# Performance work log

Measured on AMD Instinct MI355X. Metric: run time of the kernel, lower is better.

The kernel has to match this reference:

```python
import jax, jax.numpy as jnp
import numpy as np

EMBED_DIM = 2048
HEAD_DIM = 128
B, T = 4, 2048


def setup_inputs() -> dict:
    key = jax.random.key(0)
    k1, k2, k3, k4 = jax.random.split(key, 4)
    x_in = jax.random.normal(k1, (B, T, EMBED_DIM), dtype=jnp.float32)
    scale = 1.0 / np.sqrt(EMBED_DIM)
    Wq = jax.random.normal(k2, (EMBED_DIM, HEAD_DIM), dtype=jnp.float32) * scale
    Wk = jax.random.normal(k3, (EMBED_DIM, HEAD_DIM), dtype=jnp.float32) * scale
    Wv = jax.random.normal(k4, (EMBED_DIM, HEAD_DIM), dtype=jnp.float32) * scale
    return {"x_in": x_in, "Wq": Wq, "Wk": Wk, "Wv": Wv}


def reference(x_in, Wq, Wk, Wv):
    # x_in: [B, T, E]; projections (Linear, no bias)
    q = jnp.einsum('bte,ed->btd', x_in, Wq)  # [B,T,D]
    k = jnp.einsum('bte,ed->btd', x_in, Wk)
    v = jnp.einsum('bte,ed->btd', x_in, Wv)
    t = x_in.shape[1]
    d = Wq.shape[1]
    s = jnp.einsum('btd,bsd->bts', q, k) / jnp.sqrt(jnp.asarray(d, q.dtype))  # [B,Tq,Tk]
    # causal mask: positions with tril==0 (k index > q index) -> -inf
    causal = jnp.tril(jnp.ones((t, t), dtype=bool))
    s = jnp.where(causal, s, -jnp.inf)
    # NOTE: original module applies softmax over dim=1 (query axis), faithfully reproduced
    a = jax.nn.softmax(s, axis=1)
    z = jnp.einsum('bts,bsd->btd', a, v)  # [B,T,D]
    return z
```

## Files before the change

### kernel.cpp

```cpp
#include <hip/hip_runtime.h>

typedef _Float16 f16x8 __attribute__((ext_vector_type(8)));
typedef float f32x4 __attribute__((ext_vector_type(4)));

#define T_DIM 2048
#define E_DIM 2048
#define D_DIM 128
#define NB 4
#define CHUNK 32
#define NCH (T_DIM / CHUNK)
#define KSP 4
#define KCH 512

__device__ __forceinline__ void gll16(const void* g, void* l) {
  __builtin_amdgcn_global_load_lds(
      (const __attribute__((address_space(1))) unsigned int*)g,
      (__attribute__((address_space(3))) unsigned int*)l, 16, 0, 0);
}


__global__ void cvt_x(const float* __restrict__ x, _Float16* __restrict__ xh) {
  size_t i = ((size_t)blockIdx.x * 256 + threadIdx.x) * 8;
  f32x4 a = *(const f32x4*)(x + i);
  f32x4 b = *(const f32x4*)(x + i + 4);
  f16x8 o;
#pragma unroll
  for (int e = 0; e < 4; ++e) { o[e] = (_Float16)a[e]; o[e + 4] = (_Float16)b[e]; }
  *(f16x8*)(xh + i) = o;
}

__global__ void cvt_w(const float* __restrict__ Wq, const float* __restrict__ Wk,
                      const float* __restrict__ Wv, _Float16* __restrict__ WhT) {
  int idx = blockIdx.x * 256 + threadIdx.x;
  int w = blockIdx.y;
  const float* W = (w == 0) ? Wq : ((w == 1) ? Wk : Wv);
  int e = idx & (E_DIM - 1), d = idx >> 11;
  WhT[(size_t)w * (D_DIM * E_DIM) + idx] = (_Float16)W[e * D_DIM + d];
}


__global__ __launch_bounds__(256) void proj_gemm(
    const _Float16* __restrict__ xh, const _Float16* __restrict__ WhT,
    _Float16* __restrict__ Ph) {
  __shared__ _Float16 As[128 * 32];
  __shared__ _Float16 Bs[128 * 32];
  const int tid = threadIdx.x, w = tid >> 6, lane = tid & 63;
  const int wr = w >> 1, wc = w & 1, quad = lane >> 4, l16 = lane & 15;
  const int t0 = blockIdx.x * 128;
  const int wsel = blockIdx.y, ks = blockIdx.z;
  const _Float16* A = xh;
  const _Float16* B = WhT + (size_t)wsel * (D_DIM * E_DIM);
  const int srow = lane >> 2, scol = (lane & 3) * 8;
  f32x4 acc[4][4] = {};
  for (int k0 = ks * KCH; k0 < ks * KCH + KCH; k0 += 32) {
    __syncthreads();
#pragma unroll
    for (int q = 0; q < 2; ++q) {
      int rbase = w * 32 + q * 16;
      gll16(A + (size_t)(t0 + rbase + srow) * E_DIM + k0 + scol, As + rbase * 32);
      gll16(B + (size_t)(rbase + srow) * E_DIM + k0 + scol, Bs + rbase * 32);
    }
    __syncthreads();
    f16x8 af[4], bf[4];
#pragma unroll
    for (int i = 0; i < 4; ++i)
      af[i] = *(const f16x8*)(As + (wr * 64 + i * 16 + l16) * 32 + quad * 8);
#pragma unroll
    for (int j = 0; j < 4; ++j)
      bf[j] = *(const f16x8*)(Bs + (wc * 64 + j * 16 + l16) * 32 + quad * 8);
#pragma unroll
    for (int i = 0; i < 4; ++i)
#pragma unroll
      for (int j = 0; j < 4; ++j)
        acc[i][j] = __builtin_amdgcn_mfma_f32_16x16x32_f16(af[i], bf[j], acc[i][j], 0, 0, 0);
  }
  _Float16* P = Ph + ((size_t)(ks * 3 + wsel) << 20);
#pragma unroll
  for (int i = 0; i < 4; ++i)
#pragma unroll
    for (int j = 0; j < 4; ++j) {
      int n = wc * 64 + j * 16 + l16;
#pragma unroll
      for (int r = 0; r < 4; ++r) {
        int t = t0 + wr * 64 + i * 16 + quad * 4 + r;
        _Float16 h = (_Float16)acc[i][j][r];
        if (wsel < 2) P[(size_t)t * D_DIM + n] = h;
        else P[((size_t)(t >> 11) * D_DIM + n) * T_DIM + (t & (T_DIM - 1))] = h;
      }
    }
}


__global__ void proj_reduce(const _Float16* __restrict__ Ph, _Float16* __restrict__ Qh,
                            _Float16* __restrict__ Kh, _Float16* __restrict__ VT) {
  size_t u = ((size_t)blockIdx.x * 256 + threadIdx.x) * 8;
  int mat = (int)(u >> 20);
  size_t rem = u & ((1u << 20) - 1);
  float s[8] = {};
#pragma unroll
  for (int ks = 0; ks < KSP; ++ks) {
    f16x8 p = *(const f16x8*)(Ph + ((size_t)(ks * 3 + mat) << 20) + rem);
#pragma unroll
    for (int e = 0; e < 8; ++e) s[e] += (float)p[e];
  }
  f16x8 o;
#pragma unroll
  for (int e = 0; e < 8; ++e) o[e] = (_Float16)s[e];
  _Float16* dst = (mat == 0) ? Qh : ((mat == 1) ? Kh : VT);
  *(f16x8*)(dst + rem) = o;
}


__global__ __launch_bounds__(256) void s_gemm(const _Float16* __restrict__ Qh,
                                              const _Float16* __restrict__ Kh,
                                              _Float16* __restrict__ S) {
  if (blockIdx.y > blockIdx.x) return;
  __shared__ _Float16 As[128 * 32];
  __shared__ _Float16 Bs[128 * 32];
  const int tid = threadIdx.x, w = tid >> 6, lane = tid & 63;
  const int wr = w >> 1, wc = w & 1, quad = lane >> 4, l16 = lane & 15;
  const int t0 = blockIdx.x * 128, s0 = blockIdx.y * 128, b = blockIdx.z;
  const _Float16* A = Qh + (size_t)b * T_DIM * D_DIM;
  const _Float16* B = Kh + (size_t)b * T_DIM * D_DIM;
  const int srow = lane >> 2, scol = (lane & 3) * 8;
  f32x4 acc[4][4] = {};
  for (int k0 = 0; k0 < D_DIM; k0 += 32) {
    __syncthreads();
#pragma unroll
    for (int q = 0; q < 2; ++q) {
      int rbase = w * 32 + q * 16;
      gll16(A + (size_t)(t0 + rbase + srow) * D_DIM + k0 + scol, As + rbase * 32);
      gll16(B + (size_t)(s0 + rbase + srow) * D_DIM + k0 + scol, Bs + rbase * 32);
    }
    __syncthreads();
    f16x8 af[4], bf[4];
#pragma unroll
    for (int i = 0; i < 4; ++i)
      af[i] = *(const f16x8*)(As + (wr * 64 + i * 16 + l16) * 32 + quad * 8);
#pragma unroll
    for (int j = 0; j < 4; ++j)
      bf[j] = *(const f16x8*)(Bs + (wc * 64 + j * 16 + l16) * 32 + quad * 8);
#pragma unroll
    for (int i = 0; i < 4; ++i)
#pragma unroll
      for (int j = 0; j < 4; ++j)
        acc[i][j] = __builtin_amdgcn_mfma_f32_16x16x32_f16(af[i], bf[j], acc[i][j], 0, 0, 0);
  }
  _Float16* Sb = S + (size_t)b * T_DIM * T_DIM;
  const float scale = 0.08838834764831845f;
#pragma unroll
  for (int i = 0; i < 4; ++i)
#pragma unroll
    for (int j = 0; j < 4; ++j) {
      int s = s0 + wc * 64 + j * 16 + l16;
#pragma unroll
      for (int r = 0; r < 4; ++r) {
        int t = t0 + wr * 64 + i * 16 + quad * 4 + r;
        float v = acc[i][j][r] * scale;
        _Float16 h = (s > t) ? (_Float16)(-__builtin_inff()) : (_Float16)v;
        Sb[(size_t)t * T_DIM + s] = h;
      }
    }
}


__global__ __launch_bounds__(256) void part_stats(const _Float16* __restrict__ S,
                                                  float* __restrict__ Pm,
                                                  float* __restrict__ Pl) {
  const int ch = blockIdx.x, b = blockIdx.y;
  const int tbase = ch * CHUNK;
  const int s = blockIdx.z * 256 + threadIdx.x;
  const _Float16* Sb = S + (size_t)b * T_DIM * T_DIM;
  float m = -__builtin_inff(), l = 0.f;
  if (tbase + CHUNK - 1 >= s) {
    float v[CHUNK];
#pragma unroll
    for (int r = 0; r < CHUNK; ++r) {
      int t = tbase + r;
      v[r] = (t >= s) ? (float)Sb[(size_t)t * T_DIM + s] : -__builtin_inff();
      m = fmaxf(m, v[r]);
    }
#pragma unroll
    for (int r = 0; r < CHUNK; ++r) l += __expf(v[r] - m);
  }
  Pm[((size_t)ch * NB + b) * T_DIM + s] = m;
  Pl[((size_t)ch * NB + b) * T_DIM + s] = l;
}


__device__ __forceinline__ void merge_stat(float& m, float& l, float pm, float pl) {
  if (pm != -__builtin_inff()) {
    float nm = fmaxf(m, pm);
    l = l * __expf(m - nm) + pl * __expf(pm - nm);
    m = nm;
  }
}

__global__ __launch_bounds__(256) void comb_stats(const float* __restrict__ Pm,
                                                  const float* __restrict__ Pl,
                                                  float* __restrict__ M,
                                                  float* __restrict__ L) {
  __shared__ float sM[8][32];
  __shared__ float sL[8][32];
  const int g = threadIdx.x >> 5, sl = threadIdx.x & 31;
  const int c = blockIdx.x * 32 + sl;
  const int b = c >> 11, s = c & (T_DIM - 1);
  float m = -__builtin_inff(), l = 0.f;
#pragma unroll
  for (int k = 0; k < NCH / 8; ++k) {
    int ch = g * 8 + k;
    if (ch * CHUNK + CHUNK - 1 >= s) {
      size_t idx = ((size_t)ch * NB + b) * T_DIM + s;
      merge_stat(m, l, Pm[idx], Pl[idx]);
    }
  }
  sM[g][sl] = m;
  sL[g][sl] = l;
  __syncthreads();
  if (threadIdx.x < 32) {
    const int c2 = blockIdx.x * 32 + threadIdx.x;
    float fm = -__builtin_inff(), fl = 0.f;
#pragma unroll
    for (int gg = 0; gg < 8; ++gg) merge_stat(fm, fl, sM[gg][threadIdx.x], sL[gg][threadIdx.x]);
    M[c2] = fm;
    L[c2] = 1.f / fl;
  }
}


__global__ __launch_bounds__(256) void av_gemm(const _Float16* __restrict__ S,
                                               const _Float16* __restrict__ VT,
                                               const float* __restrict__ M,
                                               const float* __restrict__ L,
                                               float* __restrict__ Zp) {
  const int t0 = blockIdx.x * 128, b = blockIdx.y, ks = blockIdx.z;
  const int Kmax = t0 + 128;
  const int Kstart = ks * KCH;
  if (Kstart >= Kmax) return;
  const int Kend = (Kstart + KCH < Kmax) ? (Kstart + KCH) : Kmax;
  __shared__ _Float16 As[128 * 32];
  __shared__ _Float16 Bs[128 * 32];
  __shared__ float Ms[KCH];
  __shared__ float Ls[KCH];
  const int tid = threadIdx.x, w = tid >> 6, lane = tid & 63;
  const int wr = w >> 1, wc = w & 1, quad = lane >> 4, l16 = lane & 15;
  const _Float16* Sb = S + (size_t)b * T_DIM * T_DIM;
  const _Float16* Vb = VT + (size_t)b * D_DIM * T_DIM;
  for (int i = tid; i < Kend - Kstart; i += 256) {
    Ms[i] = M[b * T_DIM + Kstart + i];
    Ls[i] = L[b * T_DIM + Kstart + i];
  }
  const int srow = lane >> 2, scol = (lane & 3) * 8;
  f32x4 acc[4][4] = {};
  for (int k0 = Kstart; k0 < Kend; k0 += 32) {
    __syncthreads();
#pragma unroll
    for (int q = 0; q < 2; ++q) {
      int u = q * 256 + tid;
      int row = u >> 2, c8 = (u & 3) * 8;
      int sc = k0 + c8;
      f16x8 v = *(const f16x8*)(Sb + (size_t)(t0 + row) * T_DIM + sc);
      f16x8 o;
#pragma unroll
      for (int e = 0; e < 8; ++e) {
        int li = sc + e - Kstart;
        float a = __expf((float)v[e] - Ms[li]) * Ls[li];
        o[e] = (_Float16)a;
      }
      *(f16x8*)(As + row * 32 + c8) = o;
      int rbase = w * 32 + q * 16;
      gll16(Vb + (size_t)(rbase + srow) * T_DIM + k0 + scol, Bs + rbase * 32);
    }
    __syncthreads();
    f16x8 af[4], bf[4];
#pragma unroll
    for (int i = 0; i < 4; ++i)
      af[i] = *(const f16x8*)(As + (wr * 64 + i * 16 + l16) * 32 + quad * 8);
#pragma unroll
    for (int j = 0; j < 4; ++j)
      bf[j] = *(const f16x8*)(Bs + (wc * 64 + j * 16 + l16) * 32 + quad * 8);
#pragma unroll
    for (int i = 0; i < 4; ++i)
#pragma unroll
      for (int j = 0; j < 4; ++j)
        acc[i][j] = __builtin_amdgcn_mfma_f32_16x16x32_f16(af[i], bf[j], acc[i][j], 0, 0, 0);
  }
  float* Zb = Zp + (((size_t)ks * NB + b) * T_DIM) * D_DIM;
#pragma unroll
  for (int i = 0; i < 4; ++i)
#pragma unroll
    for (int j = 0; j < 4; ++j) {
      int n = wc * 64 + j * 16 + l16;
#pragma unroll
      for (int r = 0; r < 4; ++r) {
        int t = t0 + wr * 64 + i * 16 + quad * 4 + r;
        Zb[(size_t)t * D_DIM + n] = acc[i][j][r];
      }
    }
}


__global__ void z_reduce(const float* __restrict__ Zp, float* __restrict__ Z) {
  size_t flat = ((size_t)blockIdx.x * 256 + threadIdx.x) * 4;
  int t = (int)((flat >> 7) & (T_DIM - 1));
  int ns = ((t >> 7) + 4) >> 2;
  f32x4 s = {};
  for (int ks = 0; ks < ns; ++ks) {
    f32x4 p = *(const f32x4*)(Zp + ((size_t)ks * NB * T_DIM * D_DIM) + flat);
    s += p;
  }
  *(f32x4*)(Z + flat) = s;
}


extern "C" void kernel_launch(void* const* d_in, const int* in_sizes, int n_in,
                              void* d_out, int out_size, void* d_ws, size_t ws_size,
                              hipStream_t stream) {
  const float* x = (const float*)d_in[0];
  const float* Wq = (const float*)d_in[1];
  const float* Wk = (const float*)d_in[2];
  const float* Wv = (const float*)d_in[3];
  char* ws = (char*)d_ws;
  _Float16* xh = (_Float16*)(ws);
  float* Zp = (float*)(ws);
  _Float16* WhT = (_Float16*)(ws + 33554432);
  _Float16* Qh = (_Float16*)(ws + 35127296);
  _Float16* Kh = (_Float16*)(ws + 37224448);
  _Float16* VT = (_Float16*)(ws + 39321600);
  _Float16* S = (_Float16*)(ws + 41418752);
  _Float16* Ph = (_Float16*)(ws + 41418752);
  float* M = (float*)(ws + 74973184);
  float* L = (float*)(ws + 75005952);
  float* Pm = (float*)(ws + 75038720);
  float* Pl = (float*)(ws + 77135872);
  float* Z = (float*)d_out;

  cvt_x<<<8192, 256, 0, stream>>>(x, xh);
  cvt_w<<<dim3(1024, 3), 256, 0, stream>>>(Wq, Wk, Wv, WhT);
  proj_gemm<<<dim3(64, 3, KSP), 256, 0, stream>>>(xh, WhT, Ph);
  proj_reduce<<<1536, 256, 0, stream>>>(Ph, Qh, Kh, VT);
  s_gemm<<<dim3(16, 16, 4), 256, 0, stream>>>(Qh, Kh, S);
  part_stats<<<dim3(NCH, NB, 8), 256, 0, stream>>>(S, Pm, Pl);
  comb_stats<<<256, 256, 0, stream>>>(Pm, Pl, M, L);
  av_gemm<<<dim3(16, 4, KSP), 256, 0, stream>>>(S, VT, M, L, Zp);
  z_reduce<<<1024, 256, 0, stream>>>(Zp, Z);
}
```

Baseline: 193.6 us.

## Fuse x conversion into projection GEMM and softmax stats into S GEMM epilogue

New measurement: 178.4 us. -7.8%, faster.

```diff
diff --git a/kernel.cpp b/kernel.cpp
--- a/kernel.cpp
+++ b/kernel.cpp
@@ -7,10 +7,12 @@
 #define E_DIM 2048
 #define D_DIM 128
 #define NB 4
-#define CHUNK 32
-#define NCH (T_DIM / CHUNK)
-#define KSP 4
-#define KCH 512
+#define KSP_P 4
+#define KCH_P 512
+#define KSP_A 8
+#define KCH_A 256
+#define CH2 64
+#define NCH2 (T_DIM / CH2)
 
 __device__ __forceinline__ void gll16(const void* g, void* l) {
   __builtin_amdgcn_global_load_lds(
@@ -18,16 +20,14 @@
       (__attribute__((address_space(3))) unsigned int*)l, 16, 0, 0);
 }
 
-
-__global__ void cvt_x(const float* __restrict__ x, _Float16* __restrict__ xh) {
-  size_t i = ((size_t)blockIdx.x * 256 + threadIdx.x) * 8;
-  f32x4 a = *(const f32x4*)(x + i);
-  f32x4 b = *(const f32x4*)(x + i + 4);
-  f16x8 o;
-#pragma unroll
-  for (int e = 0; e < 4; ++e) { o[e] = (_Float16)a[e]; o[e + 4] = (_Float16)b[e]; }
-  *(f16x8*)(xh + i) = o;
-}
+__device__ __forceinline__ void merge_stat(float& m, float& l, float pm, float pl) {
+  if (pm != -__builtin_inff()) {
+    float nm = fmaxf(m, pm);
+    l = l * __expf(m - nm) + pl * __expf(pm - nm);
+    m = nm;
+  }
+}
+
 
 __global__ void cvt_w(const float* __restrict__ Wq, const float* __restrict__ Wk,
                       const float* __restrict__ Wv, _Float16* __restrict__ WhT) {
@@ -40,7 +40,7 @@
 
 
 __global__ __launch_bounds__(256) void proj_gemm(
-    const _Float16* __restrict__ xh, const _Float16* __restrict__ WhT,
+    const float* __restrict__ x, const _Float16* __restrict__ WhT,
     _Float16* __restrict__ Ph) {
   __shared__ _Float16 As[128 * 32];
   __shared__ _Float16 Bs[128 * 32];
@@ -48,17 +48,23 @@
   const int wr = w >> 1, wc = w & 1, quad = lane >> 4, l16 = lane & 15;
   const int t0 = blockIdx.x * 128;
   const int wsel = blockIdx.y, ks = blockIdx.z;
-  const _Float16* A = xh;
   const _Float16* B = WhT + (size_t)wsel * (D_DIM * E_DIM);
   const int srow = lane >> 2, scol = (lane & 3) * 8;
   f32x4 acc[4][4] = {};
-  for (int k0 = ks * KCH; k0 < ks * KCH + KCH; k0 += 32) {
+  for (int k0 = ks * KCH_P; k0 < ks * KCH_P + KCH_P; k0 += 32) {
     __syncthreads();
 #pragma unroll
     for (int q = 0; q < 2; ++q) {
       int rbase = w * 32 + q * 16;
-      gll16(A + (size_t)(t0 + rbase + srow) * E_DIM + k0 + scol, As + rbase * 32);
-      gll16(B + (size_t)(rbase + srow) * E_DIM + k0 + scol, Bs + rbase * 32);
+      int row = rbase + srow;
+      const float* xp = x + (size_t)(t0 + row) * E_DIM + k0 + scol;
+      f32x4 a0 = *(const f32x4*)xp;
+      f32x4 a1 = *(const f32x4*)(xp + 4);
+      f16x8 o;
+#pragma unroll
+      for (int e = 0; e < 4; ++e) { o[e] = (_Float16)a0[e]; o[e + 4] = (_Float16)a1[e]; }
+      *(f16x8*)(As + row * 32 + scol) = o;
+      gll16(B + (size_t)row * E_DIM + k0 + scol, Bs + rbase * 32);
     }
     __syncthreads();
     f16x8 af[4], bf[4];
@@ -98,7 +104,7 @@
   size_t rem = u & ((1u << 20) - 1);
   float s[8] = {};
 #pragma unroll
-  for (int ks = 0; ks < KSP; ++ks) {
+  for (int ks = 0; ks < KSP_P; ++ks) {
     f16x8 p = *(const f16x8*)(Ph + ((size_t)(ks * 3 + mat) << 20) + rem);
 #pragma unroll
     for (int e = 0; e < 8; ++e) s[e] += (float)p[e];
@@ -113,13 +119,19 @@
 
 __global__ __launch_bounds__(256) void s_gemm(const _Float16* __restrict__ Qh,
                                               const _Float16* __restrict__ Kh,
-                                              _Float16* __restrict__ S) {
-  if (blockIdx.y > blockIdx.x) return;
+                                              _Float16* __restrict__ S,
+                                              float* __restrict__ Pm,
+                                              float* __restrict__ Pl) {
+  int idx = blockIdx.x;
+  int xt = (int)((sqrtf(8.f * idx + 1.f) - 1.f) * 0.5f);
+  while ((xt + 1) * (xt + 2) / 2 <= idx) ++xt;
+  while (xt * (xt + 1) / 2 > idx) --xt;
+  int yt = idx - xt * (xt + 1) / 2;
   __shared__ _Float16 As[128 * 32];
   __shared__ _Float16 Bs[128 * 32];
   const int tid = threadIdx.x, w = tid >> 6, lane = tid & 63;
   const int wr = w >> 1, wc = w & 1, quad = lane >> 4, l16 = lane & 15;
-  const int t0 = blockIdx.x * 128, s0 = blockIdx.y * 128, b = blockIdx.z;
+  const int t0 = xt * 128, s0 = yt * 128, b = blockIdx.y;
   const _Float16* A = Qh + (size_t)b * T_DIM * D_DIM;
   const _Float16* B = Kh + (size_t)b * T_DIM * D_DIM;
   const int srow = lane >> 2, scol = (lane & 3) * 8;
@@ -148,53 +160,45 @@
   }
   _Float16* Sb = S + (size_t)b * T_DIM * T_DIM;
   const float scale = 0.08838834764831845f;
-#pragma unroll
-  for (int i = 0; i < 4; ++i)
-#pragma unroll
-    for (int j = 0; j < 4; ++j) {
-      int s = s0 + wc * 64 + j * 16 + l16;
+  const float NEG = -__builtin_inff();
+#pragma unroll
+  for (int j = 0; j < 4; ++j) {
+    const int s = s0 + wc * 64 + j * 16 + l16;
+    float m = NEG;
+#pragma unroll
+    for (int i = 0; i < 4; ++i)
 #pragma unroll
       for (int r = 0; r < 4; ++r) {
         int t = t0 + wr * 64 + i * 16 + quad * 4 + r;
-        float v = acc[i][j][r] * scale;
-        _Float16 h = (s > t) ? (_Float16)(-__builtin_inff()) : (_Float16)v;
-        Sb[(size_t)t * T_DIM + s] = h;
+        float v = (s > t) ? NEG : acc[i][j][r] * scale;
+        Sb[(size_t)t * T_DIM + s] = (_Float16)v;
+        m = fmaxf(m, v);
       }
-    }
-}
-
-
-__global__ __launch_bounds__(256) void part_stats(const _Float16* __restrict__ S,
-                                                  float* __restrict__ Pm,
-                                                  float* __restrict__ Pl) {
-  const int ch = blockIdx.x, b = blockIdx.y;
-  const int tbase = ch * CHUNK;
-  const int s = blockIdx.z * 256 + threadIdx.x;
-  const _Float16* Sb = S + (size_t)b * T_DIM * T_DIM;
-  float m = -__builtin_inff(), l = 0.f;
-  if (tbase + CHUNK - 1 >= s) {
-    float v[CHUNK];
-#pragma unroll
-    for (int r = 0; r < CHUNK; ++r) {
-      int t = tbase + r;
-      v[r] = (t >= s) ? (float)Sb[(size_t)t * T_DIM + s] : -__builtin_inff();
-      m = fmaxf(m, v[r]);
-    }
-#pragma unroll
-    for (int r = 0; r < CHUNK; ++r) l += __expf(v[r] - m);
-  }
-  Pm[((size_t)ch * NB + b) * T_DIM + s] = m;
-  Pl[((size_t)ch * NB + b) * T_DIM + s] = l;
-}
-
-
-__device__ __forceinline__ void merge_stat(float& m, float& l, float pm, float pl) {
-  if (pm != -__builtin_inff()) {
-    float nm = fmaxf(m, pm);
-    l = l * __expf(m - nm) + pl * __expf(pm - nm);
-    m = nm;
-  }
-}
+    float l = 0.f;
+    if (m != NEG) {
+#pragma unroll
+      for (int i = 0; i < 4; ++i)
+#pragma unroll
+        for (int r = 0; r < 4; ++r) {
+          int t = t0 + wr * 64 + i * 16 + quad * 4 + r;
+          float v = (s > t) ? NEG : acc[i][j][r] * scale;
+          l += __expf(v - m);
+        }
+    }
+#pragma unroll
+    for (int d = 16; d <= 32; d <<= 1) {
+      float pm = __shfl_xor(m, d, 64);
+      float pl = __shfl_xor(l, d, 64);
+      merge_stat(m, l, pm, pl);
+    }
+    if (quad == 0) {
+      int c = 2 * xt + wr;
+      Pm[((size_t)c * NB + b) * T_DIM + s] = m;
+      Pl[((size_t)c * NB + b) * T_DIM + s] = l;
+    }
+  }
+}
+
 
 __global__ __launch_bounds__(256) void comb_stats(const float* __restrict__ Pm,
                                                   const float* __restrict__ Pl,
@@ -207,9 +211,9 @@
   const int b = c >> 11, s = c & (T_DIM - 1);
   float m = -__builtin_inff(), l = 0.f;
 #pragma unroll
-  for (int k = 0; k < NCH / 8; ++k) {
-    int ch = g * 8 + k;
-    if (ch * CHUNK + CHUNK - 1 >= s) {
+  for (int k = 0; k < NCH2 / 8; ++k) {
+    int ch = g * (NCH2 / 8) + k;
+    if (ch >= (s >> 6)) {
       size_t idx = ((size_t)ch * NB + b) * T_DIM + s;
       merge_stat(m, l, Pm[idx], Pl[idx]);
     }
@@ -235,13 +239,13 @@
                                                float* __restrict__ Zp) {
   const int t0 = blockIdx.x * 128, b = blockIdx.y, ks = blockIdx.z;
   const int Kmax = t0 + 128;
-  const int Kstart = ks * KCH;
+  const int Kstart = ks * KCH_A;
   if (Kstart >= Kmax) return;
-  const int Kend = (Kstart + KCH < Kmax) ? (Kstart + KCH) : Kmax;
+  const int Kend = (Kstart + KCH_A < Kmax) ? (Kstart + KCH_A) : Kmax;
   __shared__ _Float16 As[128 * 32];
   __shared__ _Float16 Bs[128 * 32];
-  __shared__ float Ms[KCH];
-  __shared__ float Ls[KCH];
+  __shared__ float Ms[KCH_A];
+  __shared__ float Ls[KCH_A];
   const int tid = threadIdx.x, w = tid >> 6, lane = tid & 63;
   const int wr = w >> 1, wc = w & 1, quad = lane >> 4, l16 = lane & 15;
   const _Float16* Sb = S + (size_t)b * T_DIM * T_DIM;
@@ -285,7 +289,7 @@
       for (int j = 0; j < 4; ++j)
         acc[i][j] = __builtin_amdgcn_mfma_f32_16x16x32_f16(af[i], bf[j], acc[i][j], 0, 0, 0);
   }
-  float* Zb = Zp + (((size_t)ks * NB + b) * T_DIM) * D_DIM;
+  float* Zb = Zp + ((size_t)ks * NB + b) * T_DIM * D_DIM;
 #pragma unroll
   for (int i = 0; i < 4; ++i)
 #pragma unroll
@@ -303,7 +307,7 @@
 __global__ void z_reduce(const float* __restrict__ Zp, float* __restrict__ Z) {
   size_t flat = ((size_t)blockIdx.x * 256 + threadIdx.x) * 4;
   int t = (int)((flat >> 7) & (T_DIM - 1));
-  int ns = ((t >> 7) + 4) >> 2;
+  int ns = ((t >> 7) + 2) >> 1;
   f32x4 s = {};
   for (int ks = 0; ks < ns; ++ks) {
     f32x4 p = *(const f32x4*)(Zp + ((size_t)ks * NB * T_DIM * D_DIM) + flat);
@@ -321,7 +325,6 @@
   const float* Wk = (const float*)d_in[2];
   const float* Wv = (const float*)d_in[3];
   char* ws = (char*)d_ws;
-  _Float16* xh = (_Float16*)(ws);
   float* Zp = (float*)(ws);
   _Float16* WhT = (_Float16*)(ws + 33554432);
   _Float16* Qh = (_Float16*)(ws + 35127296);
@@ -332,16 +335,14 @@
   float* M = (float*)(ws + 74973184);
   float* L = (float*)(ws + 75005952);
   float* Pm = (float*)(ws + 75038720);
-  float* Pl = (float*)(ws + 77135872);
+  float* Pl = (float*)(ws + 76087296);
   float* Z = (float*)d_out;
 
-  cvt_x<<<8192, 256, 0, stream>>>(x, xh);
   cvt_w<<<dim3(1024, 3), 256, 0, stream>>>(Wq, Wk, Wv, WhT);
-  proj_gemm<<<dim3(64, 3, KSP), 256, 0, stream>>>(xh, WhT, Ph);
+  proj_gemm<<<dim3(64, 3, KSP_P), 256, 0, stream>>>(x, WhT, Ph);
   proj_reduce<<<1536, 256, 0, stream>>>(Ph, Qh, Kh, VT);
-  s_gemm<<<dim3(16, 16, 4), 256, 0, stream>>>(Qh, Kh, S);
-  part_stats<<<dim3(NCH, NB, 8), 256, 0, stream>>>(S, Pm, Pl);
+  s_gemm<<<dim3(136, 4), 256, 0, stream>>>(Qh, Kh, S, Pm, Pl);
   comb_stats<<<256, 256, 0, stream>>>(Pm, Pl, M, L);
-  av_gemm<<<dim3(16, 4, KSP), 256, 0, stream>>>(S, VT, M, L, Zp);
+  av_gemm<<<dim3(16, 4, KSP_A), 256, 0, stream>>>(S, VT, M, L, Zp);
   z_reduce<<<1024, 256, 0, stream>>>(Zp, Z);
 }
```
